# Optimization experiments

Hardware: AMD Instinct MI355X
Metric: run time of the kernel (lower is better)

The kernel has to match this reference:

```python
import jax, jax.numpy as jnp
import numpy as np
import math

RATIOS = [2, 4, 8, 16]   # attn_aggr_ratio per path
HEAD_DIM = 64
EPS = 1e-5               # BatchNorm1d eps (eval mode, running stats)


def _bn(x, g, b, m, v):
    # x: (N, C, L); per-channel eval-mode BatchNorm1d
    inv = g / jnp.sqrt(v + EPS)
    return x * inv[None, :, None] + (b - m * inv)[None, :, None]


def _conv1(x, W, b=None):
    # 1x1 Conv1d == channel matmul. x: (N, Cin, L), W: (Cout, Cin)
    y = jnp.einsum('ncl,dc->ndl', x, W)
    if b is not None:
        y = y + b[None, :, None]
    return y


def setup_inputs() -> dict:
    key = jax.random.key(0)
    ks = iter(jax.random.split(key, 16))
    N, C, L = 8, 512, 3072
    P, d = 4, C // 4
    FF = 4 * C
    w = lambda shape: jax.random.normal(next(ks), shape, dtype=jnp.float32) * 0.05
    inp = {'x': jax.random.normal(next(ks), (N, C, L), dtype=jnp.float32)}
    for nm in ('norm1', 'norm2'):
        inp[nm + '_g'] = jnp.ones((C,), jnp.float32)
        inp[nm + '_b'] = jnp.zeros((C,), jnp.float32)
        inp[nm + '_m'] = jnp.zeros((C,), jnp.float32)
        inp[nm + '_v'] = jnp.ones((C,), jnp.float32)
    for nm in ('Wq', 'Wk', 'Wv', 'Wo', 'Wp'):
        inp[nm] = w((P, d, d))
    for nm in ('bq', 'bk', 'bv', 'bo'):
        inp[nm] = jnp.zeros((P, d), jnp.float32)
    for nm in ('ag', 'an'):  # aggr-block BN and pre-KV BN, per path
        inp[nm + '_g'] = jnp.ones((P, d), jnp.float32)
        inp[nm + '_b'] = jnp.zeros((P, d), jnp.float32)
        inp[nm + '_m'] = jnp.zeros((P, d), jnp.float32)
        inp[nm + '_v'] = jnp.ones((P, d), jnp.float32)
    inp['W1'] = w((FF, C)); inp['b1'] = jnp.zeros((FF,), jnp.float32)
    inp['W2'] = w((C, FF)); inp['b2'] = jnp.zeros((C,), jnp.float32)
    return inp


def reference(x, norm1_g, norm1_b, norm1_m, norm1_v,
              Wq, bq, Wk, bk, Wv, bv, Wo, bo, Wp,
              ag_g, ag_b, ag_m, ag_v, an_g, an_b, an_m, an_v,
              norm2_g, norm2_b, norm2_m, norm2_v,
              W1, b1, W2, b2):
    N, C, L = x.shape
    P = len(RATIOS)
    d = C // P
    h = _bn(x, norm1_g, norm1_b, norm1_m, norm1_v)
    outs = []
    for i, r in enumerate(RATIOS):  # small fixed set of paths
        xi = h[:, i * d:(i + 1) * d, :]                       # (N, d, L)
        q = _conv1(xi, Wq[i], bq[i])                          # (N, d, L)
        # local aware aggregation: avg_pool + max_pool (L divisible by r)
        xp = xi.reshape(N, d, L // r, r)
        xa = xp.mean(-1) + xp.max(-1)                         # (N, d, L/r)
        xa = _bn(_conv1(xa, Wp[i]), ag_g[i], ag_b[i], ag_m[i], ag_v[i])
        xa = _bn(xa, an_g[i], an_b[i], an_m[i], an_v[i])
        k = _conv1(xa, Wk[i], bk[i])
        v = _conv1(xa, Wv[i], bv[i])
        Nh = d // HEAD_DIM
        Lk = L // r
        qh = q.reshape(N, Nh, HEAD_DIM, L) / math.sqrt(HEAD_DIM)
        kh = k.reshape(N, Nh, HEAD_DIM, Lk)
        vh = v.reshape(N, Nh, HEAD_DIM, Lk)
        attn = jax.nn.softmax(jnp.einsum('nhel,nhem->nhlm', qh, kh), axis=-1)
        o = jnp.einsum('nhlm,nhem->nhel', attn, vh).reshape(N, d, L)
        outs.append(_conv1(o, Wo[i], bo[i]))
    x = x + jnp.concatenate(outs, axis=1)                     # residual
    h2 = _bn(x, norm2_g, norm2_b, norm2_m, norm2_v)
    m = jax.nn.gelu(_conv1(h2, W1, b1))
    m = _conv1(m, W2, b2)
    return x + m
```

## Files before the change

### kernel.cpp

```cpp
#include <hip/hip_runtime.h>
#include <math.h>

#define EPS 1e-5f

#define F_BIAS  1
#define F_DBN   2
#define F_GELU  4
#define F_RESID 8

typedef __attribute__((ext_vector_type(8))) __bf16 bf16x8;
typedef __attribute__((ext_vector_type(4))) float f32x4;
typedef __attribute__((ext_vector_type(8))) unsigned short u16x8;

__device__ __forceinline__ unsigned int pack2bf(float a, float b) {
    unsigned short ua = __builtin_bit_cast(unsigned short, (__bf16)a);
    unsigned short ub = __builtin_bit_cast(unsigned short, (__bf16)b);
    return (unsigned int)ua | ((unsigned int)ub << 16);
}

__device__ __forceinline__ void gload_lds16(const unsigned short* g, unsigned short* l) {
    __builtin_amdgcn_global_load_lds(
        (const __attribute__((address_space(1))) unsigned int*)g,
        (__attribute__((address_space(3))) unsigned int*)l,
        16, 0, 0);
}

__device__ __forceinline__ float gelu_f(float u) {
    float s = u * u;
    float w = u * fmaf(s, 0.0713548162726f, 1.59576912161f);
    float e = __expf(-w);
    return u * __builtin_amdgcn_rcpf(1.f + e);
}

__device__ __constant__ int c_LKS[4]  = {1536, 768, 384, 192};
__device__ __constant__ int c_OFFB[4] = {0, 1572864, 2359296, 2752512};

__global__ __launch_bounds__(256) void wcvt_kernel(
    const float* __restrict__ Wq, const float* __restrict__ Wk,
    const float* __restrict__ Wv, const float* __restrict__ Wo,
    const float* __restrict__ Wp, const float* __restrict__ W1,
    const float* __restrict__ W2, unsigned short* __restrict__ dst)
{
    const int WSZ = 65536;
    const int FSZ = 1048576;
    int i4 = blockIdx.x * blockDim.x + threadIdx.x;
    long long i = (long long)i4 * 4;
    const long long total = 5LL * WSZ + 2LL * FSZ;
    if (i >= total) return;
    #pragma unroll
    for (int j = 0; j < 4; ++j) {
        long long idx = i + j;
        float v;
        if      (idx < WSZ)            v = Wq[idx];
        else if (idx < 2 * WSZ)        v = Wk[idx - WSZ];
        else if (idx < 3 * WSZ)        v = Wv[idx - 2 * WSZ];
        else if (idx < 4 * WSZ)        v = Wo[idx - 3 * WSZ];
        else if (idx < 5 * WSZ)        v = Wp[idx - 4 * WSZ];
        else if (idx < 5 * WSZ + FSZ)  v = W1[idx - 5 * WSZ];
        else                           v = W2[idx - 5 * WSZ - FSZ];
        dst[idx] = __builtin_bit_cast(unsigned short, (__bf16)v);
    }
}

__global__ __launch_bounds__(256) void bn_transpose_kernel(
    const float* __restrict__ x,
    const float* __restrict__ g, const float* __restrict__ b,
    const float* __restrict__ bm, const float* __restrict__ bvv,
    unsigned short* __restrict__ hT, int C, int L)
{
    __shared__ float ps[64][65];
    const int l0 = blockIdx.x * 64, ct = blockIdx.y, n = blockIdx.z;
    const int tid = threadIdx.x;
    const int c = tid >> 2, q = tid & 3;
    const int cg = ct * 64 + c;
    float inv = g[cg] * rsqrtf(bvv[cg] + EPS);
    float add = b[cg] - bm[cg] * inv;
    const float* xp = x + ((size_t)n * C + cg) * L + l0 + q * 16;
    #pragma unroll
    for (int s = 0; s < 4; ++s) {
        float4 vv = *(const float4*)&xp[s * 4];
        ps[c][q * 16 + s * 4 + 0] = fmaf(vv.x, inv, add);
        ps[c][q * 16 + s * 4 + 1] = fmaf(vv.y, inv, add);
        ps[c][q * 16 + s * 4 + 2] = fmaf(vv.z, inv, add);
        ps[c][q * 16 + s * 4 + 3] = fmaf(vv.w, inv, add);
    }
    __syncthreads();
    #pragma unroll
    for (int j = 0; j < 2; ++j) {
        int row = (tid >> 3) + 32 * j;
        int cc0 = (tid & 7) * 8;
        unsigned int w0 = pack2bf(ps[cc0 + 0][row], ps[cc0 + 1][row]);
        unsigned int w1 = pack2bf(ps[cc0 + 2][row], ps[cc0 + 3][row]);
        unsigned int w2 = pack2bf(ps[cc0 + 4][row], ps[cc0 + 5][row]);
        unsigned int w3 = pack2bf(ps[cc0 + 6][row], ps[cc0 + 7][row]);
        *(uint4*)&hT[((size_t)n * L + l0 + row) * C + ct * 64 + cc0] =
            make_uint4(w0, w1, w2, w3);
    }
}

__global__ __launch_bounds__(256) void pool_bn_all_kernel(
    const float* __restrict__ x,
    const float* __restrict__ g, const float* __restrict__ b,
    const float* __restrict__ bm, const float* __restrict__ bvv,
    unsigned short* __restrict__ xa0T_all, int C, int L)
{
    const int p = blockIdx.z & 3;
    const int n = blockIdx.z >> 2;
    const int Lk = c_LKS[p];
    const int lk0 = blockIdx.x * 64;
    if (lk0 >= Lk) return;
    const int r = L / Lk;
    const int ct = blockIdx.y;
    __shared__ float ps[64][65];
    const int tid = threadIdx.x;
    const int c = tid >> 2, q = tid & 3;
    const int cg = p * 128 + ct * 64 + c;
    float inv = g[cg] * rsqrtf(bvv[cg] + EPS);
    float add = b[cg] - bm[cg] * inv;
    const float* xp = x + ((size_t)n * C + cg) * L;
    float rinv = 1.0f / (float)r;
    #pragma unroll
    for (int s = 0; s < 16; ++s) {
        int lk = q * 16 + s;
        const float* base = xp + (size_t)(lk0 + lk) * r;
        float sum = 0.f, mx = -INFINITY;
        for (int j = 0; j < r; j += 2) {
            float2 vv = *(const float2*)&base[j];
            float t0 = fmaf(vv.x, inv, add);
            float t1 = fmaf(vv.y, inv, add);
            sum += t0 + t1;
            mx = fmaxf(mx, fmaxf(t0, t1));
        }
        ps[c][lk] = sum * rinv + mx;
    }
    __syncthreads();
    unsigned short* dst = xa0T_all + c_OFFB[p];
    #pragma unroll
    for (int j = 0; j < 2; ++j) {
        int row = (tid >> 3) + 32 * j;
        int cc0 = (tid & 7) * 8;
        unsigned int w0 = pack2bf(ps[cc0 + 0][row], ps[cc0 + 1][row]);
        unsigned int w1 = pack2bf(ps[cc0 + 2][row], ps[cc0 + 3][row]);
        unsigned int w2 = pack2bf(ps[cc0 + 4][row], ps[cc0 + 5][row]);
        unsigned int w3 = pack2bf(ps[cc0 + 6][row], ps[cc0 + 7][row]);
        *(uint4*)&dst[((size_t)n * Lk + lk0 + row) * 128 + ct * 64 + cc0] =
            make_uint4(w0, w1, w2, w3);
    }
}

template<int OMODE>
__global__ __launch_bounds__(256) void gemm_bf(
    const unsigned short* __restrict__ A, const unsigned short* __restrict__ BT,
    int M, int K, int Npos, int ldBT, long long strideBT,
    const float* __restrict__ bias, float oscale, int flags,
    const float* __restrict__ g1, const float* __restrict__ b1p,
    const float* __restrict__ m1p, const float* __restrict__ v1p,
    const float* __restrict__ g2, const float* __restrict__ b2p,
    const float* __restrict__ m2p, const float* __restrict__ v2p,
    float* __restrict__ outN, long long strideN,
    const float* __restrict__ resid, long long strideR,
    unsigned short* __restrict__ outT, int ldT, int moff, long long strideT,
    int gKoff)
{
    __shared__ __align__(16) unsigned short As[2][128][32];
    __shared__ __align__(16) unsigned short Bs[2][128][32];

    const int tid = threadIdx.x;

    const int gdx = gridDim.x, gdy = gridDim.y;
    const int nwg = gdx * gdy * gridDim.z;
    int bid = blockIdx.x + gdx * (blockIdx.y + gdy * blockIdx.z);
    {
        int q = nwg >> 3, rr = nwg & 7;
        int xcd = bid & 7, idx = bid >> 3;
        bid = (xcd < rr ? xcd * (q + 1) : rr * (q + 1) + (xcd - rr) * q) + idx;
    }
    const int bx = bid % gdx;
    const int by = (bid / gdx) % gdy;
    const int bz = bid / (gdx * gdy);

    const int m0 = by * 128;
    const int p0 = bx * 128;
    const unsigned short* Bn = BT + (size_t)bz * strideBT
                              + (size_t)(m0 >> 7) * gKoff;

    const int wave = tid >> 6;
    const int lane = tid & 63;
    const int qcol = lane & 15;
    const int hi   = lane >> 4;
    const int wr   = wave >> 1;
    const int wc   = wave & 1;
    const int lrow = lane >> 2;
    const int lseg = (lane & 3) * 8;

    const unsigned short* aR0 = A + (size_t)(m0 + wave * 32 + lrow) * K + lseg;
    const unsigned short* aR1 = aR0 + (size_t)16 * K;
    int pr0 = p0 + wave * 32 + lrow;      if (pr0 > Npos - 1) pr0 = Npos - 1;
    int pr1 = p0 + wave * 32 + 16 + lrow; if (pr1 > Npos - 1) pr1 = Npos - 1;
    const unsigned short* bR0 = Bn + (size_t)pr0 * ldBT + lseg;
    const unsigned short* bR1 = Bn + (size_t)pr1 * ldBT + lseg;
    unsigned short* ldsA0 = &As[0][wave * 32][0];
    unsigned short* ldsA1 = &As[0][wave * 32 + 16][0];
    unsigned short* ldsB0 = &Bs[0][wave * 32][0];
    unsigned short* ldsB1 = &Bs[0][wave * 32 + 16][0];
    const int bufStride = 128 * 32;

    auto STAGE = [&](int b, int t) {
        const int ko = t * 32;
        gload_lds16(aR0 + ko, ldsA0 + b * bufStride);
        gload_lds16(aR1 + ko, ldsA1 + b * bufStride);
        gload_lds16(bR0 + ko, ldsB0 + b * bufStride);
        gload_lds16(bR1 + ko, ldsB1 + b * bufStride);
    };

    f32x4 acc[4][4] = {};
    const int nt = K >> 5;

    STAGE(0, 0);
    STAGE(1, 1);

    auto MFMA_STEP = [&](int b) {
        bf16x8 af[4], bfr[4];
        #pragma unroll
        for (int mi = 0; mi < 4; ++mi)
            af[mi] = *(const bf16x8*)&As[b][wr * 64 + mi * 16 + qcol][hi * 8];
        #pragma unroll
        for (int ni = 0; ni < 4; ++ni)
            bfr[ni] = *(const bf16x8*)&Bs[b][wc * 64 + ni * 16 + qcol][hi * 8];
        #pragma unroll
        for (int mi = 0; mi < 4; ++mi)
            #pragma unroll
            for (int ni = 0; ni < 4; ++ni)
                acc[mi][ni] = __builtin_amdgcn_mfma_f32_16x16x32_bf16(
                    af[mi], bfr[ni], acc[mi][ni], 0, 0, 0);
    };

    int cur = 0;
    for (int t = 0; t < nt - 1; ++t) {
        asm volatile("s_waitcnt vmcnt(4)" ::: "memory");
        __builtin_amdgcn_s_barrier();
        MFMA_STEP(cur);
        __builtin_amdgcn_s_barrier();
        if (t + 2 < nt) STAGE(cur, t + 2);
        cur ^= 1;
    }
    asm volatile("s_waitcnt vmcnt(0)" ::: "memory");
    __builtin_amdgcn_s_barrier();
    MFMA_STEP(cur);

    float* Cn = outN + (size_t)bz * strideN;
    const float* Rn = resid + (size_t)bz * strideR;
    unsigned short* Tn = outT + (size_t)bz * strideT;

    #pragma unroll
    for (int mi = 0; mi < 4; ++mi) {
        const int mb = m0 + wr * 64 + mi * 16 + hi * 4;
        float4 bv4 = make_float4(0.f, 0.f, 0.f, 0.f);
        if (flags & F_BIAS) bv4 = *(const float4*)&bias[mb];
        float s1[4], t1[4];
        if ((flags & F_DBN) || OMODE == 3) {
            float4 gg = *(const float4*)&g1[mb];
            float4 bb = *(const float4*)&b1p[mb];
            float4 mm = *(const float4*)&m1p[mb];
            float4 vv = *(const float4*)&v1p[mb];
            float gga[4] = {gg.x, gg.y, gg.z, gg.w};
            float bba[4] = {bb.x, bb.y, bb.z, bb.w};
            float mma[4] = {mm.x, mm.y, mm.z, mm.w};
            float vva[4] = {vv.x, vv.y, vv.z, vv.w};
            #pragma unroll
            for (int r2 = 0; r2 < 4; ++r2) {
                float iv = gga[r2] * rsqrtf(vva[r2] + EPS);
                s1[r2] = iv; t1[r2] = bba[r2] - mma[r2] * iv;
            }
        }
        float s2[4], t2[4];
        if (flags & F_DBN) {
            float4 gg = *(const float4*)&g2[mb];
            float4 bb = *(const float4*)&b2p[mb];
            float4 mm = *(const float4*)&m2p[mb];
            float4 vv = *(const float4*)&v2p[mb];
            float gga[4] = {gg.x, gg.y, gg.z, gg.w};
            float bba[4] = {bb.x, bb.y, bb.z, bb.w};
            float mma[4] = {mm.x, mm.y, mm.z, mm.w};
            float vva[4] = {vv.x, vv.y, vv.z, vv.w};
            #pragma unroll
            for (int r2 = 0; r2 < 4; ++r2) {
                float iv = gga[r2] * rsqrtf(vva[r2] + EPS);
                s2[r2] = iv; t2[r2] = bba[r2] - mma[r2] * iv;
            }
        }
        const float ba[4] = {bv4.x, bv4.y, bv4.z, bv4.w};
        #pragma unroll
        for (int ni = 0; ni < 4; ++ni) {
            const int cp = p0 + wc * 64 + ni * 16 + qcol;
            if (cp >= Npos) continue;
            float vals[4];
            #pragma unroll
            for (int r2 = 0; r2 < 4; ++r2) {
                float val = (acc[mi][ni][r2] + ba[r2]) * oscale;
                if (flags & F_DBN) {
                    val = fmaf(val, s1[r2], t1[r2]);
                    val = fmaf(val, s2[r2], t2[r2]);
                }
                if (flags & F_GELU) val = gelu_f(val);
                vals[r2] = val;
            }
            if (OMODE == 0 || OMODE == 3) {
                #pragma unroll
                for (int r2 = 0; r2 < 4; ++r2) {
                    size_t off = (size_t)(mb + r2) * Npos + cp;
                    float v = vals[r2];
                    if (flags & F_RESID) v += Rn[off];
                    Cn[off] = v;
                    vals[r2] = v;
                }
            }
            if (OMODE == 1) {
                *(uint2*)&Tn[(size_t)cp * ldT + moff + mb] =
                    make_uint2(pack2bf(vals[0], vals[1]), pack2bf(vals[2], vals[3]));
            }
            if (OMODE == 2) {
                #pragma unroll
                for (int r2 = 0; r2 < 4; ++r2)
                    Tn[(size_t)(mb + r2) * Npos + cp] =
                        __builtin_bit_cast(unsigned short, (__bf16)vals[r2]);
            }
            if (OMODE == 3) {
                float a0 = fmaf(vals[0], s1[0], t1[0]);
                float a1 = fmaf(vals[1], s1[1], t1[1]);
                float a2 = fmaf(vals[2], s1[2], t1[2]);
                float a3 = fmaf(vals[3], s1[3], t1[3]);
                *(uint2*)&Tn[(size_t)cp * ldT + moff + mb] =
                    make_uint2(pack2bf(a0, a1), pack2bf(a2, a3));
            }
        }
    }
}

template<int OMODE, int FLAGS>
__global__ __launch_bounds__(512, 1) void gemm_bf256(
    const unsigned short* __restrict__ A, const unsigned short* __restrict__ BT,
    int K, int Npos, int ldBT, long long strideBT,
    const float* __restrict__ bias,
    float* __restrict__ outN, long long strideN,
    const float* __restrict__ resid, long long strideR,
    unsigned short* __restrict__ outT, int ldT, long long strideT)
{
    __shared__ __align__(16) unsigned short As[4][256][32];
    __shared__ __align__(16) unsigned short Bs[4][256][32];

    const int tid = threadIdx.x;

    const int gdx = gridDim.x, gdy = gridDim.y;
    const int nwg = gdx * gdy * gridDim.z;
    int bid = blockIdx.x + gdx * (blockIdx.y + gdy * blockIdx.z);
    {
        int q = nwg >> 3, rr = nwg & 7;
        int xcd = bid & 7, idx = bid >> 3;
        bid = (xcd < rr ? xcd * (q + 1) : rr * (q + 1) + (xcd - rr) * q) + idx;
    }
    const int bx = bid % gdx;
    const int by = (bid / gdx) % gdy;
    const int bz = bid / (gdx * gdy);

    const int m0 = by * 256;
    const int p0 = bx * 256;
    const unsigned short* Bn = BT + (size_t)bz * strideBT;

    const int wave = tid >> 6;
    const int lane = tid & 63;
    const int qcol = lane & 15;
    const int hi   = lane >> 4;
    const int wr   = wave >> 2;
    const int wc   = wave & 3;

    const int lrow4 = lane >> 2;
    const int sseg  = ((lane & 3) ^ (lrow4 & 3)) * 8;

    const unsigned short* aS0 = A + (size_t)(m0 + wave * 32 + lrow4) * K + sseg;
    const unsigned short* aS1 = aS0 + (size_t)16 * K;
    const unsigned short* bS0 = Bn + (size_t)(p0 + wave * 32 + lrow4) * ldBT + sseg;
    const unsigned short* bS1 = bS0 + (size_t)16 * ldBT;
    unsigned short* ldsA0 = &As[0][wave * 32][0];
    unsigned short* ldsA1 = &As[0][wave * 32 + 16][0];
    unsigned short* ldsB0 = &Bs[0][wave * 32][0];
    unsigned short* ldsB1 = &Bs[0][wave * 32 + 16][0];
    const int bufStride = 256 * 32;

    auto STAGE = [&](int b, int t) {
        const int ko = t * 32;
        gload_lds16(aS0 + ko, ldsA0 + b * bufStride);
        gload_lds16(aS1 + ko, ldsA1 + b * bufStride);
        gload_lds16(bS0 + ko, ldsB0 + b * bufStride);
        gload_lds16(bS1 + ko, ldsB1 + b * bufStride);
    };

    const int xr = (hi ^ (qcol & 3)) * 8;

    f32x4 acc[8][4] = {};
    const int nt = K >> 5;

    STAGE(0, 0); STAGE(1, 1); STAGE(2, 2);

    auto MFMA_STEP = [&](int b) {
        bf16x8 af[8], bfr[4];
        #pragma unroll
        for (int mi = 0; mi < 8; ++mi)
            af[mi] = *(const bf16x8*)&As[b][wr * 128 + mi * 16 + qcol][xr];
        #pragma unroll
        for (int ni = 0; ni < 4; ++ni)
            bfr[ni] = *(const bf16x8*)&Bs[b][wc * 64 + ni * 16 + qcol][xr];
        #pragma unroll
        for (int mi = 0; mi < 8; ++mi)
            #pragma unroll
            for (int ni = 0; ni < 4; ++ni)
                acc[mi][ni] = __builtin_amdgcn_mfma_f32_16x16x32_bf16(
                    af[mi], bfr[ni], acc[mi][ni], 0, 0, 0);
    };

    for (int t = 0; t < nt; ++t) {
        const int rem = nt - t;
        if (rem >= 3)      { asm volatile("s_waitcnt vmcnt(8)" ::: "memory"); }
        else if (rem == 2) { asm volatile("s_waitcnt vmcnt(4)" ::: "memory"); }
        else               { asm volatile("s_waitcnt vmcnt(0)" ::: "memory"); }
        __builtin_amdgcn_s_barrier();
        __builtin_amdgcn_s_setprio(1);
        MFMA_STEP(t & 3);
        __builtin_amdgcn_s_setprio(0);
        __builtin_amdgcn_s_barrier();
        if (t + 3 < nt) STAGE((t + 3) & 3, t + 3);
    }

    float* Cn = outN + (size_t)bz * strideN;
    const float* Rn = resid + (size_t)bz * strideR;
    unsigned short* Tn = outT + (size_t)bz * strideT;

    #pragma unroll
    for (int mi = 0; mi < 8; ++mi) {
        const int mb = m0 + wr * 128 + mi * 16 + hi * 4;
        float ba[4] = {0.f, 0.f, 0.f, 0.f};
        if (FLAGS & F_BIAS) {
            float4 bv4 = *(const float4*)&bias[mb];
            ba[0] = bv4.x; ba[1] = bv4.y; ba[2] = bv4.z; ba[3] = bv4.w;
        }
        #pragma unroll
        for (int ni = 0; ni < 4; ++ni) {
            const int cp = p0 + wc * 64 + ni * 16 + qcol;
            float vals[4];
            #pragma unroll
            for (int r2 = 0; r2 < 4; ++r2) {
                float val = acc[mi][ni][r2] + ba[r2];
                if (FLAGS & F_GELU) val = gelu_f(val);
                vals[r2] = val;
            }
            if (OMODE == 0) {
                #pragma unroll
                for (int r2 = 0; r2 < 4; ++r2) {
                    size_t off = (size_t)(mb + r2) * Npos + cp;
                    float v = vals[r2];
                    if (FLAGS & F_RESID) v += Rn[off];
                    Cn[off] = v;
                }
            } else {
                *(uint2*)&Tn[(size_t)cp * ldT + mb] =
                    make_uint2(pack2bf(vals[0], vals[1]), pack2bf(vals[2], vals[3]));
            }
        }
    }
}

template<int MODE>
__global__ __launch_bounds__(256) void gemm_path(
    const unsigned short* __restrict__ A0, const unsigned short* __restrict__ A1,
    const unsigned short* __restrict__ Bsrc,
    const float* __restrict__ bias0, const float* __restrict__ bias1,
    const float* __restrict__ agg, const float* __restrict__ agb,
    const float* __restrict__ agm, const float* __restrict__ agv,
    const float* __restrict__ ang, const float* __restrict__ anb,
    const float* __restrict__ anm, const float* __restrict__ anv,
    unsigned short* __restrict__ out0, unsigned short* __restrict__ out1)
{
    __shared__ __align__(16) unsigned short As[2][128][32];
    __shared__ __align__(16) unsigned short Bs[2][128][32];

    const int tid = threadIdx.x;
    const int gdx = gridDim.x, gdy = gridDim.y;
    const int nwg = gdx * gdy * gridDim.z;
    int bid = blockIdx.x + gdx * (blockIdx.y + gdy * blockIdx.z);
    {
        int q = nwg >> 3, rr = nwg & 7;
        int xcd = bid & 7, idx = bid >> 3;
        bid = (xcd < rr ? xcd * (q + 1) : rr * (q + 1) + (xcd - rr) * q) + idx;
    }
    const int bx = bid % gdx;
    const int by = (bid / gdx) % gdy;
    const int bz = bid / (gdx * gdy);

    int p, px;
    if      (bx < 12) { p = 0; px = bx; }
    else if (bx < 18) { p = 1; px = bx - 12; }
    else if (bx < 21) { p = 2; px = bx - 18; }
    else              { p = 3; px = bx - 21; }
    const int Lk = c_LKS[p];
    const int offb = c_OFFB[p];
    const int c0 = p * 128;
    const int p0 = px * 128;
    const int K = 128;

    const unsigned short* A = (MODE == 1 && by == 1 ? A1 : A0) + p * 16384;
    const unsigned short* Bn = Bsrc + offb + (size_t)bz * Lk * 128;

    const int wave = tid >> 6;
    const int lane = tid & 63;
    const int qcol = lane & 15;
    const int hi   = lane >> 4;
    const int wr   = wave >> 1;
    const int wc   = wave & 1;
    const int lrow = lane >> 2;
    const int lseg = (lane & 3) * 8;

    const unsigned short* aR0 = A + (size_t)(wave * 32 + lrow) * K + lseg;
    const unsigned short* aR1 = aR0 + (size_t)16 * K;
    int pr0 = p0 + wave * 32 + lrow;      if (pr0 > Lk - 1) pr0 = Lk - 1;
    int pr1 = p0 + wave * 32 + 16 + lrow; if (pr1 > Lk - 1) pr1 = Lk - 1;
    const unsigned short* bR0 = Bn + (size_t)pr0 * 128 + lseg;
    const unsigned short* bR1 = Bn + (size_t)pr1 * 128 + lseg;
    unsigned short* ldsA0 = &As[0][wave * 32][0];
    unsigned short* ldsA1 = &As[0][wave * 32 + 16][0];
    unsigned short* ldsB0 = &Bs[0][wave * 32][0];
    unsigned short* ldsB1 = &Bs[0][wave * 32 + 16][0];
    const int bufStride = 128 * 32;

    auto STAGE = [&](int b, int t) {
        const int ko = t * 32;
        gload_lds16(aR0 + ko, ldsA0 + b * bufStride);
        gload_lds16(aR1 + ko, ldsA1 + b * bufStride);
        gload_lds16(bR0 + ko, ldsB0 + b * bufStride);
        gload_lds16(bR1 + ko, ldsB1 + b * bufStride);
    };

    f32x4 acc[4][4] = {};
    STAGE(0, 0);
    STAGE(1, 1);

    auto MFMA_STEP = [&](int b) {
        bf16x8 af[4], bfr[4];
        #pragma unroll
        for (int mi = 0; mi < 4; ++mi)
            af[mi] = *(const bf16x8*)&As[b][wr * 64 + mi * 16 + qcol][hi * 8];
        #pragma unroll
        for (int ni = 0; ni < 4; ++ni)
            bfr[ni] = *(const bf16x8*)&Bs[b][wc * 64 + ni * 16 + qcol][hi * 8];
        #pragma unroll
        for (int mi = 0; mi < 4; ++mi)
            #pragma unroll
            for (int ni = 0; ni < 4; ++ni)
                acc[mi][ni] = __builtin_amdgcn_mfma_f32_16x16x32_bf16(
                    af[mi], bfr[ni], acc[mi][ni], 0, 0, 0);
    };

    int cur = 0;
    const int nt = 4;
    for (int t = 0; t < nt - 1; ++t) {
        asm volatile("s_waitcnt vmcnt(4)" ::: "memory");
        __builtin_amdgcn_s_barrier();
        MFMA_STEP(cur);
        __builtin_amdgcn_s_barrier();
        if (t + 2 < nt) STAGE(cur, t + 2);
        cur ^= 1;
    }
    asm volatile("s_waitcnt vmcnt(0)" ::: "memory");
    __builtin_amdgcn_s_barrier();
    MFMA_STEP(cur);

    const bool isV = (MODE == 1 && by == 1);
    unsigned short* Tn = (isV ? out1 : out0) + offb + (size_t)bz * Lk * 128;
    const float* bias = (MODE == 0) ? nullptr : (by == 0 ? bias0 : bias1);

    #pragma unroll
    for (int mi = 0; mi < 4; ++mi) {
        const int mb = wr * 64 + mi * 16 + hi * 4;
        float ba[4] = {0.f, 0.f, 0.f, 0.f};
        if (MODE == 1) {
            float4 bv4 = *(const float4*)&bias[c0 + mb];
            ba[0] = bv4.x; ba[1] = bv4.y; ba[2] = bv4.z; ba[3] = bv4.w;
        }
        float s1[4], t1[4], s2[4], t2[4];
        if (MODE == 0) {
            #pragma unroll
            for (int r2 = 0; r2 < 4; ++r2) {
                int gm = c0 + mb + r2;
                float i1 = agg[gm] * rsqrtf(agv[gm] + EPS);
                s1[r2] = i1; t1[r2] = agb[gm] - agm[gm] * i1;
                float i2 = ang[gm] * rsqrtf(anv[gm] + EPS);
                s2[r2] = i2; t2[r2] = anb[gm] - anm[gm] * i2;
            }
        }
        #pragma unroll
        for (int ni = 0; ni < 4; ++ni) {
            const int cp = p0 + wc * 64 + ni * 16 + qcol;
            if (cp >= Lk) continue;
            float vals[4];
            #pragma unroll
            for (int r2 = 0; r2 < 4; ++r2) {
                float val = acc[mi][ni][r2] + ba[r2];
                if (MODE == 0) {
                    val = fmaf(val, s1[r2], t1[r2]);
                    val = fmaf(val, s2[r2], t2[r2]);
                }
                vals[r2] = val;
            }
            if (!isV) {
                *(uint2*)&Tn[(size_t)cp * 128 + mb] =
                    make_uint2(pack2bf(vals[0], vals[1]), pack2bf(vals[2], vals[3]));
            } else {
                #pragma unroll
                for (int r2 = 0; r2 < 4; ++r2)
                    Tn[(size_t)(mb + r2) * Lk + cp] =
                        __builtin_bit_cast(unsigned short, (__bf16)vals[r2]);
            }
        }
    }
}

__global__ __launch_bounds__(256) void attn_bf_all_kernel(
    const unsigned short* __restrict__ qT, const unsigned short* __restrict__ kT_all,
    const unsigned short* __restrict__ vN_all, unsigned short* __restrict__ obT,
    int L)
{
    const int p = blockIdx.z;
    const int Lk = c_LKS[p];
    const int offb = c_OFFB[p];
    const int l0 = blockIdx.x * 64;
    const int nh = blockIdx.y;
    const int n = nh >> 1, h = nh & 1;
    const unsigned short* qn = qT + (size_t)n * L * 512 + p * 128 + h * 64;
    const unsigned short* kn = kT_all + offb + (size_t)n * Lk * 128 + h * 64;
    const unsigned short* vn = vN_all + offb + ((size_t)n * 128 + h * 64) * Lk;
    unsigned short*       on = obT + (size_t)n * L * 512 + p * 128 + h * 64;

    __shared__ __align__(16) unsigned short Ks[2][64][64];
    __shared__ __align__(16) unsigned short Vs[2][64][64];
    __shared__ __align__(16) unsigned short Ps[4][16][72];

    const int tid = threadIdx.x;
    const int wave = tid >> 6;
    const int lane = tid & 63;
    const int qcol = lane & 15;
    const int hi   = lane >> 4;
    const int ql   = wave * 16 + qcol;

    const int srow = lane >> 3;
    const int sxor = (lane & 7) ^ srow;
    const unsigned short* kS0 = kn + (size_t)(wave * 16 + srow) * 128 + sxor * 8;
    const unsigned short* kS1 = kn + (size_t)(wave * 16 + 8 + srow) * 128 + sxor * 8;
    const unsigned short* vS0 = vn + (size_t)(wave * 16 + srow) * Lk + sxor * 8;
    const unsigned short* vS1 = vn + (size_t)(wave * 16 + 8 + srow) * Lk + sxor * 8;
    unsigned short* ldsK0 = &Ks[0][wave * 16][0];
    unsigned short* ldsK1 = &Ks[0][wave * 16 + 8][0];
    unsigned short* ldsV0 = &Vs[0][wave * 16][0];
    unsigned short* ldsV1 = &Vs[0][wave * 16 + 8][0];
    const int bufStride = 64 * 64;

    auto STAGE = [&](int b, int t) {
        const int mc = t * 64;
        gload_lds16(kS0 + (size_t)mc * 128, ldsK0 + b * bufStride);
        gload_lds16(kS1 + (size_t)mc * 128, ldsK1 + b * bufStride);
        gload_lds16(vS0 + mc, ldsV0 + b * bufStride);
        gload_lds16(vS1 + mc, ldsV1 + b * bufStride);
    };

    const int x0 = (hi ^ (qcol & 7)) * 8;
    const int x1 = x0 ^ 32;

    bf16x8 qf0 = *(const bf16x8*)&qn[(size_t)(l0 + ql) * 512 + hi * 8];
    bf16x8 qf1 = *(const bf16x8*)&qn[(size_t)(l0 + ql) * 512 + 32 + hi * 8];

    f32x4 o_acc[4] = {};
    float mrow = -INFINITY, lrow = 0.f;
    const int nt = Lk >> 6;

    STAGE(0, 0);
    STAGE(1, 1);

    auto COMPUTE = [&](int b) {
        f32x4 sacc[4];
        #pragma unroll
        for (int kt = 0; kt < 4; ++kt) {
            bf16x8 k0 = *(const bf16x8*)&Ks[b][kt * 16 + qcol][x0];
            bf16x8 k1 = *(const bf16x8*)&Ks[b][kt * 16 + qcol][x1];
            f32x4 a = {};
            a = __builtin_amdgcn_mfma_f32_16x16x32_bf16(k0, qf0, a, 0, 0, 0);
            a = __builtin_amdgcn_mfma_f32_16x16x32_bf16(k1, qf1, a, 0, 0, 0);
            sacc[kt] = a;
        }
        float m0 = fmaxf(fmaxf(sacc[0][0], sacc[0][1]), fmaxf(sacc[0][2], sacc[0][3]));
        float m1 = fmaxf(fmaxf(sacc[1][0], sacc[1][1]), fmaxf(sacc[1][2], sacc[1][3]));
        float m2 = fmaxf(fmaxf(sacc[2][0], sacc[2][1]), fmaxf(sacc[2][2], sacc[2][3]));
        float m3 = fmaxf(fmaxf(sacc[3][0], sacc[3][1]), fmaxf(sacc[3][2], sacc[3][3]));
        float cm = fmaxf(fmaxf(m0, m1), fmaxf(m2, m3));
        cm = fmaxf(cm, __shfl_xor(cm, 16));
        cm = fmaxf(cm, __shfl_xor(cm, 32));
        float nm = fmaxf(mrow, cm);
        float alpha = __expf(mrow - nm);
        float csum = 0.f;
        unsigned int pw[4][2];
        #pragma unroll
        for (int kt = 0; kt < 4; ++kt) {
            float p0 = __expf(sacc[kt][0] - nm);
            float p1 = __expf(sacc[kt][1] - nm);
            float p2 = __expf(sacc[kt][2] - nm);
            float p3 = __expf(sacc[kt][3] - nm);
            csum += (p0 + p1) + (p2 + p3);
            pw[kt][0] = pack2bf(p0, p1);
            pw[kt][1] = pack2bf(p2, p3);
        }
        csum += __shfl_xor(csum, 16);
        csum += __shfl_xor(csum, 32);
        lrow = lrow * alpha + csum;
        mrow = nm;

        #pragma unroll
        for (int kt = 0; kt < 4; ++kt)
            *(uint2*)&Ps[wave][qcol][kt * 16 + hi * 4] =
                make_uint2(pw[kt][0], pw[kt][1]);

        #pragma unroll
        for (int et = 0; et < 4; ++et)
            #pragma unroll
            for (int r2 = 0; r2 < 4; ++r2) o_acc[et][r2] *= alpha;

        bf16x8 pf0 = *(const bf16x8*)&Ps[wave][qcol][hi * 8];
        bf16x8 pf1 = *(const bf16x8*)&Ps[wave][qcol][hi * 8 + 32];
        #pragma unroll
        for (int et = 0; et < 4; ++et) {
            bf16x8 v0 = *(const bf16x8*)&Vs[b][et * 16 + qcol][x0];
            bf16x8 v1 = *(const bf16x8*)&Vs[b][et * 16 + qcol][x1];
            o_acc[et] = __builtin_amdgcn_mfma_f32_16x16x32_bf16(v0, pf0, o_acc[et], 0, 0, 0);
            o_acc[et] = __builtin_amdgcn_mfma_f32_16x16x32_bf16(v1, pf1, o_acc[et], 0, 0, 0);
        }
    };

    int cur = 0;
    for (int t = 0; t < nt - 1; ++t) {
        asm volatile("s_waitcnt vmcnt(4)" ::: "memory");
        __builtin_amdgcn_s_barrier();
        COMPUTE(cur);
        __builtin_amdgcn_s_barrier();
        if (t + 2 < nt) STAGE(cur, t + 2);
        cur ^= 1;
    }
    asm volatile("s_waitcnt vmcnt(0)" ::: "memory");
    __builtin_amdgcn_s_barrier();
    COMPUTE(cur);

    float invl = 1.f / lrow;
    #pragma unroll
    for (int et = 0; et < 4; ++et) {
        float a0 = o_acc[et][0] * invl, a1 = o_acc[et][1] * invl;
        float a2 = o_acc[et][2] * invl, a3 = o_acc[et][3] * invl;
        *(uint2*)&on[(size_t)(l0 + ql) * 512 + et * 16 + hi * 4] =
            make_uint2(pack2bf(a0, a1), pack2bf(a2, a3));
    }
}

extern "C" void kernel_launch(void* const* d_in, const int* in_sizes, int n_in,
                              void* d_out, int out_size, void* d_ws, size_t ws_size,
                              hipStream_t stream)
{
    const float* x   = (const float*)d_in[0];
    const float* n1g = (const float*)d_in[1];
    const float* n1b = (const float*)d_in[2];
    const float* n1m = (const float*)d_in[3];
    const float* n1v = (const float*)d_in[4];
    const float* n2g = (const float*)d_in[5];
    const float* n2b = (const float*)d_in[6];
    const float* n2m = (const float*)d_in[7];
    const float* n2v = (const float*)d_in[8];
    const float* Wq  = (const float*)d_in[9];
    const float* Wk  = (const float*)d_in[10];
    const float* Wv  = (const float*)d_in[11];
    const float* Wo  = (const float*)d_in[12];
    const float* Wp  = (const float*)d_in[13];
    const float* bq  = (const float*)d_in[14];
    const float* bk  = (const float*)d_in[15];
    const float* bv  = (const float*)d_in[16];
    const float* bo  = (const float*)d_in[17];
    const float* agg = (const float*)d_in[18];
    const float* agb = (const float*)d_in[19];
    const float* agm = (const float*)d_in[20];
    const float* agv = (const float*)d_in[21];
    const float* ang = (const float*)d_in[22];
    const float* anb = (const float*)d_in[23];
    const float* anm = (const float*)d_in[24];
    const float* anv = (const float*)d_in[25];
    const float* W1  = (const float*)d_in[26];
    const float* b1  = (const float*)d_in[27];
    const float* W2  = (const float*)d_in[28];
    const float* b2  = (const float*)d_in[29];

    float* out = (float*)d_out;
    unsigned short* wsb = (unsigned short*)d_ws;

    const int N = 8, Cc = 512, L = 3072, FF = 2048;
    const int WSZ = 65536, FSZ = 1048576;
    const size_t PATHBUF = 2949120;

    unsigned short* wbf      = wsb;
    unsigned short* hT       = wbf      + 5 * WSZ + 2 * FSZ;
    unsigned short* h2T      = hT;
    unsigned short* obT      = hT       + (size_t)N * L * Cc;
    unsigned short* xa0T_all = obT      + (size_t)N * L * 512;
    unsigned short* xabT_all = xa0T_all + PATHBUF;
    unsigned short* kT_all   = xabT_all + PATHBUF;
    unsigned short* vN_all   = kT_all   + PATHBUF;
    unsigned short* m1T      = vN_all   + PATHBUF;
    unsigned short* qTall    = m1T;

    const unsigned short* WqB = wbf;
    const unsigned short* WkB = wbf + WSZ;
    const unsigned short* WvB = wbf + 2 * WSZ;
    const unsigned short* WoB = wbf + 3 * WSZ;
    const unsigned short* WpB = wbf + 4 * WSZ;
    const unsigned short* W1B = wbf + 5 * WSZ;
    const unsigned short* W2B = wbf + 5 * WSZ + FSZ;

    const float* nul = nullptr;
    float* nulf = nullptr;
    unsigned short* nulu = nullptr;

    {
        long long tot4 = (5LL * WSZ + 2LL * FSZ) / 4;
        wcvt_kernel<<<dim3((unsigned)((tot4 + 255) / 256)), dim3(256), 0, stream>>>(
            Wq, Wk, Wv, Wo, Wp, W1, W2, wbf);
    }
    bn_transpose_kernel<<<dim3(L / 64, Cc / 64, N), dim3(256), 0, stream>>>(
        x, n1g, n1b, n1m, n1v, hT, Cc, L);

    pool_bn_all_kernel<<<dim3(24, 2, N * 4), dim3(256), 0, stream>>>(
        x, n1g, n1b, n1m, n1v, xa0T_all, Cc, L);

    gemm_bf<1><<<dim3(L / 128, 4, N), dim3(256), 0, stream>>>(
        WqB, hT, 512, 128, L, Cc, (long long)L * Cc,
        bq, 0.125f, F_BIAS,
        nul, nul, nul, nul, nul, nul, nul, nul,
        nulf, 0, nul, 0, qTall, 512, 0, (long long)L * 512, 128);

    gemm_path<0><<<dim3(23, 1, N), dim3(256), 0, stream>>>(
        WpB, nulu, xa0T_all, nul, nul,
        agg, agb, agm, agv, ang, anb, anm, anv,
        xabT_all, nulu);

    gemm_path<1><<<dim3(23, 2, N), dim3(256), 0, stream>>>(
        WkB, WvB, xabT_all, bk, bv,
        nul, nul, nul, nul, nul, nul, nul, nul,
        kT_all, vN_all);

    attn_bf_all_kernel<<<dim3(L / 64, N * 2, 4), dim3(256), 0, stream>>>(
        qTall, kT_all, vN_all, obT, L);

    gemm_bf<3><<<dim3(L / 128, 4, N), dim3(256), 0, stream>>>(
        WoB, obT, 512, 128, L, 512, (long long)L * 512,
        bo, 1.f, F_BIAS | F_RESID,
        n2g, n2b, n2m, n2v,
        nul, nul, nul, nul,
        out, (long long)Cc * L,
        x, (long long)Cc * L,
        h2T, Cc, 0, (long long)L * Cc, 128);

    gemm_bf256<1, F_BIAS | F_GELU><<<dim3(L / 256, FF / 256, N), dim3(512), 0, stream>>>(
        W1B, h2T, Cc, L, Cc, (long long)L * Cc,
        b1,
        nulf, 0, nul, 0,
        m1T, FF, (long long)L * FF);

    gemm_bf256<0, F_BIAS | F_RESID><<<dim3(L / 256, Cc / 256, N), dim3(512), 0, stream>>>(
        W2B, m1T, FF, L, FF, (long long)L * FF,
        b2,
        out, (long long)Cc * L, out, (long long)Cc * L,
        nulu, 0, 0);
}
```

Baseline: 533.1 us.

## Templatize FFN GEMM tile height, use double buffering and smaller tiles for W2

```diff
diff --git a/kernel.cpp b/kernel.cpp
--- a/kernel.cpp
+++ b/kernel.cpp
@@ -337,8 +337,8 @@
     }
 }
 
-template<int OMODE, int FLAGS>
-__global__ __launch_bounds__(512, 1) void gemm_bf256(
+template<int OMODE, int FLAGS, int NMI>
+__global__ __launch_bounds__(512, 1) void gemm_ffn(
     const unsigned short* __restrict__ A, const unsigned short* __restrict__ BT,
     int K, int Npos, int ldBT, long long strideBT,
     const float* __restrict__ bias,
@@ -346,8 +346,9 @@
     const float* __restrict__ resid, long long strideR,
     unsigned short* __restrict__ outT, int ldT, long long strideT)
 {
-    __shared__ __align__(16) unsigned short As[4][256][32];
-    __shared__ __align__(16) unsigned short Bs[4][256][32];
+    const int BM = NMI * 32;
+    __shared__ __align__(16) unsigned short As[2][NMI * 32][32];
+    __shared__ __align__(16) unsigned short Bs[2][256][32];
 
     const int tid = threadIdx.x;
 
@@ -363,7 +364,7 @@
     const int by = (bid / gdx) % gdy;
     const int bz = bid / (gdx * gdy);
 
-    const int m0 = by * 256;
+    const int m0 = by * BM;
     const int p0 = bx * 256;
     const unsigned short* Bn = BT + (size_t)bz * strideBT;
 
@@ -375,69 +376,74 @@
     const int wc   = wave & 3;
 
     const int lrow4 = lane >> 2;
-    const int sseg  = ((lane & 3) ^ (lrow4 & 3)) * 8;
-
-    const unsigned short* aS0 = A + (size_t)(m0 + wave * 32 + lrow4) * K + sseg;
+    const int sseg  = (lane & 3) * 8;
+
+    const int arow = wave * (NMI * 4);
+    const unsigned short* aS0 = A + (size_t)(m0 + arow + lrow4) * K + sseg;
     const unsigned short* aS1 = aS0 + (size_t)16 * K;
     const unsigned short* bS0 = Bn + (size_t)(p0 + wave * 32 + lrow4) * ldBT + sseg;
     const unsigned short* bS1 = bS0 + (size_t)16 * ldBT;
-    unsigned short* ldsA0 = &As[0][wave * 32][0];
-    unsigned short* ldsA1 = &As[0][wave * 32 + 16][0];
+    unsigned short* ldsA0 = &As[0][arow][0];
+    unsigned short* ldsA1 = &As[0][arow + 16][0];
     unsigned short* ldsB0 = &Bs[0][wave * 32][0];
     unsigned short* ldsB1 = &Bs[0][wave * 32 + 16][0];
-    const int bufStride = 256 * 32;
+    const int aStride = BM * 32;
+    const int bStride = 256 * 32;
 
     auto STAGE = [&](int b, int t) {
         const int ko = t * 32;
-        gload_lds16(aS0 + ko, ldsA0 + b * bufStride);
-        gload_lds16(aS1 + ko, ldsA1 + b * bufStride);
-        gload_lds16(bS0 + ko, ldsB0 + b * bufStride);
-        gload_lds16(bS1 + ko, ldsB1 + b * bufStride);
+        gload_lds16(aS0 + ko, ldsA0 + b * aStride);
+        if constexpr (NMI == 8) gload_lds16(aS1 + ko, ldsA1 + b * aStride);
+        gload_lds16(bS0 + ko, ldsB0 + b * bStride);
+        gload_lds16(bS1 + ko, ldsB1 + b * bStride);
     };
-
-    const int xr = (hi ^ (qcol & 3)) * 8;
-
-    f32x4 acc[8][4] = {};
+    const int NL = (NMI == 8) ? 4 : 3;
+
+    f32x4 acc[NMI][4] = {};
     const int nt = K >> 5;
 
-    STAGE(0, 0); STAGE(1, 1); STAGE(2, 2);
+    STAGE(0, 0);
+    STAGE(1, 1);
 
     auto MFMA_STEP = [&](int b) {
-        bf16x8 af[8], bfr[4];
-        #pragma unroll
-        for (int mi = 0; mi < 8; ++mi)
-            af[mi] = *(const bf16x8*)&As[b][wr * 128 + mi * 16 + qcol][xr];
+        bf16x8 af[NMI], bfr[4];
+        #pragma unroll
+        for (int mi = 0; mi < NMI; ++mi)
+            af[mi] = *(const bf16x8*)&As[b][wr * (NMI * 16) + mi * 16 + qcol][hi * 8];
         #pragma unroll
         for (int ni = 0; ni < 4; ++ni)
-            bfr[ni] = *(const bf16x8*)&Bs[b][wc * 64 + ni * 16 + qcol][xr];
-        #pragma unroll
-        for (int mi = 0; mi < 8; ++mi)
+            bfr[ni] = *(const bf16x8*)&Bs[b][wc * 64 + ni * 16 + qcol][hi * 8];
+        #pragma unroll
+        for (int mi = 0; mi < NMI; ++mi)
             #pragma unroll
             for (int ni = 0; ni < 4; ++ni)
                 acc[mi][ni] = __builtin_amdgcn_mfma_f32_16x16x32_bf16(
                     af[mi], bfr[ni], acc[mi][ni], 0, 0, 0);
     };
 
-    for (int t = 0; t < nt; ++t) {
-        const int rem = nt - t;
-        if (rem >= 3)      { asm volatile("s_waitcnt vmcnt(8)" ::: "memory"); }
-        else if (rem == 2) { asm volatile("s_waitcnt vmcnt(4)" ::: "memory"); }
-        else               { asm volatile("s_waitcnt vmcnt(0)" ::: "memory"); }
+    int cur = 0;
+    for (int t = 0; t < nt - 1; ++t) {
+        if (NL == 4) { asm volatile("s_waitcnt vmcnt(4)" ::: "memory"); }
+        else         { asm volatile("s_waitcnt vmcnt(3)" ::: "memory"); }
         __builtin_amdgcn_s_barrier();
         __builtin_amdgcn_s_setprio(1);
-        MFMA_STEP(t & 3);
+        MFMA_STEP(cur);
         __builtin_amdgcn_s_setprio(0);
         __builtin_amdgcn_s_barrier();
-        if (t + 3 < nt) STAGE((t + 3) & 3, t + 3);
-    }
+        if (t + 2 < nt) STAGE(cur, t + 2);
+        cur ^= 1;
+    }
+    asm volatile("s_waitcnt vmcnt(0)" ::: "memory");
+    __builtin_amdgcn_s_barrier();
+    MFMA_STEP(cur);
 
     float* Cn = outN + (size_t)bz * strideN;
     const float* Rn = resid + (size_t)bz * strideR;
     unsigned short* Tn = outT + (size_t)bz * strideT;
 
     #pragma unroll
-    for (int mi = 0; mi < 8; ++mi) {
-        const int mb = m0 + wr * 128 + mi * 16 + hi * 4;
+    for (int mi = 0; mi < NMI; ++mi) {
+        const int mb = m0 + wr * (NMI * 16) + mi * 16 + hi * 4;
         float ba[4] = {0.f, 0.f, 0.f, 0.f};
         if (FLAGS & F_BIAS) {
             float4 bv4 = *(const float4*)&bias[mb];
@@ -868,13 +874,13 @@
         x, (long long)Cc * L,
         h2T, Cc, 0, (long long)L * Cc, 128);
 
-    gemm_bf256<1, F_BIAS | F_GELU><<<dim3(L / 256, FF / 256, N), dim3(512), 0, stream>>>(
+    gemm_ffn<1, F_BIAS | F_GELU, 8><<<dim3(L / 256, FF / 256, N), dim3(512), 0, stream>>>(
         W1B, h2T, Cc, L, Cc, (long long)L * Cc,
         b1,
         nulf, 0, nul, 0,
         m1T, FF, (long long)L * FF);
 
-    gemm_bf256<0, F_BIAS | F_RESID><<<dim3(L / 256, Cc / 256, N), dim3(512), 0, stream>>>(
+    gemm_ffn<0, F_BIAS | F_RESID, 4><<<dim3(L / 256, Cc / 128, N), dim3(512), 0, stream>>>(
         W2B, m1T, FF, L, FF, (long long)L * FF,
         b2,
         out, (long long)Cc * L, out, (long long)Cc * L,
```

Result: faster. 499.0 us (-6.4%).
